# Kernel tuning notes

Measured on AMD Instinct MI355X. Metric: run time of the kernel, lower is better.

The kernel has to match this reference:

```python
import jax, jax.numpy as jnp
import numpy as np

NEG_BIG = -1.0e10
LRELU_SLOPE = 0.2
N_NODES = 256  # hardcoded in the original via np.identity(256)


def setup_inputs() -> dict:
    key = jax.random.key(0)
    ks = jax.random.split(key, 7)
    B, N, F, H, F_ = 128, N_NODES, 512, 8, 64
    X = jax.random.normal(ks[0], (B, N, F), dtype=jnp.float32)
    # binary adjacency mask in {0,1}
    A = jax.random.randint(ks[1], (B, N, N), 0, 2).astype(jnp.float32)
    kernels = jax.random.normal(ks[2], (H, F, F_), dtype=jnp.float32) * 0.05
    biases = jax.random.normal(ks[3], (H, F_), dtype=jnp.float32) * 0.05
    attn_self = jax.random.normal(ks[4], (H, F_), dtype=jnp.float32) * 0.05
    attn_neigh = jax.random.normal(ks[5], (H, F_), dtype=jnp.float32) * 0.05
    alpha = jax.random.normal(ks[6], (N // 2, N // 2), dtype=jnp.float32) * 0.05
    return {"X": X, "A": A, "kernels": kernels, "biases": biases,
            "attn_self": attn_self, "attn_neigh": attn_neigh, "alpha": alpha}


def reference(X, A, kernels, biases, attn_self, attn_neigh, alpha):
    B, N, F = X.shape
    H, _, F_ = kernels.shape
    # per-head linear projection: [H,B,N,F_]
    feats = jnp.einsum('bnf,hfk->hbnk', X, kernels)
    # additive attention logits
    a_self = jnp.einsum('hbnk,hk->hbn', feats, attn_self)    # [H,B,N]
    a_neigh = jnp.einsum('hbnk,hk->hbn', feats, attn_neigh)  # [H,B,N]
    dense = a_self[..., :, None] + a_neigh[..., None, :]     # [H,B,N,N]
    dense = jnp.where(dense > 0, dense, LRELU_SLOPE * dense)  # LeakyReLU(0.2)
    dense = dense + NEG_BIG * (1.0 - A)                      # mask non-edges
    attn = jax.nn.softmax(dense, axis=-1)                    # [H,B,N,N]
    # weighted aggregation + bias (dropout is identity at inference)
    node = jnp.einsum('hbij,hbjk->hbik', attn, feats) + biases[:, None, None, :]
    # concat heads -> [B,N,H*F_], then activation (relu)
    output = jnp.transpose(node, (1, 2, 0, 3)).reshape(B, N, H * F_)
    output = jax.nn.relu(output)

    # head-averaged attention map
    view = jnp.mean(attn, axis=0)                            # [B,N,N]
    # 2x2 max pool, stride 2
    pooled = view.reshape(B, N // 2, 2, N // 2, 2).max(axis=(2, 4))  # [B,N/2,N/2]
    temp = jnp.einsum('bij,jk->bik', pooled, alpha)
    s = jnp.sum(temp, axis=(-1, -2)).reshape(B, 1)           # [B,1]
    thresh = jax.nn.sigmoid(s)                               # [B,1]
    # binarize: where((view + I) < thresh, 1, 0), per-batch scalar threshold
    eye = jnp.eye(N, dtype=view.dtype)
    dense4 = jnp.where(view + eye[None] < thresh[:, :, None],
                       jnp.ones_like(view), jnp.zeros_like(view))
    return (output, dense4)
```

## Files before the change

### kernel.cpp

```cpp
#include <hip/hip_runtime.h>
#include <hip/hip_bf16.h>
#include <cstdio>
#include <math.h>


typedef __attribute__((ext_vector_type(8))) short   s16x8;
typedef __attribute__((ext_vector_type(8))) __bf16  bf16x8;
typedef __attribute__((ext_vector_type(4))) float   fx4;

#define FADD __fadd_rn
#define FMUL __fmul_rn
#define FSUB __fsub_rn
#define FDIV __fdiv_rn
#define MASKC (-9999998976.0f)

__device__ __forceinline__ fx4 mfma_bf16_16x16x32(s16x8 a, s16x8 b, fx4 c) {
    return __builtin_amdgcn_mfma_f32_16x16x32_bf16(
        __builtin_bit_cast(bf16x8, a), __builtin_bit_cast(bf16x8, b), c, 0, 0, 0);
}
__device__ __forceinline__ unsigned short f2bf(float f) {
    unsigned int x = __builtin_bit_cast(unsigned int, f);
    unsigned int lsb = (x >> 16) & 1u;
    x += 0x7fffu + lsb;
    return (unsigned short)(x >> 16);
}
__device__ __forceinline__ unsigned int pack2(float a, float b) {
    return (unsigned int)f2bf(a) | ((unsigned int)f2bf(b) << 16);
}
__device__ __forceinline__ float expf_cr(float x) {
    return (float)exp((double)x);
}

__device__ float pw128(const float* a) {
    float c[16];
#pragma unroll
    for (int l = 0; l < 16; ++l) {
        float t0 = FADD(FADD(a[l], a[16 + l]), FADD(a[32 + l], a[48 + l]));
        float t1 = FADD(FADD(a[64 + l], a[80 + l]), FADD(a[96 + l], a[112 + l]));
        c[l] = FADD(t0, t1);
    }
    float d[8], e[4], f[2];
#pragma unroll
    for (int l = 0; l < 8; ++l) d[l] = FADD(c[l], c[l + 8]);
#pragma unroll
    for (int l = 0; l < 4; ++l) e[l] = FADD(d[l], d[l + 4]);
#pragma unroll
    for (int l = 0; l < 2; ++l) f[l] = FADD(e[l], e[l + 2]);
    return FADD(f[0], f[1]);
}

__global__ __launch_bounds__(256) void repack_w(const float* __restrict__ kern,
                                                unsigned short* __restrict__ wkt) {
    int t = blockIdx.x * 256 + threadIdx.x;
    int n = t >> 9, f = t & 511;
    int h = n >> 6, k = n & 63;
    wkt[t] = f2bf(kern[(h * 512 + f) * 64 + k]);
}

__global__ __launch_bounds__(256) void repack_k32(const float* __restrict__ kern,
                                                  float* __restrict__ kern_r) {
    int t = blockIdx.x * 256 + threadIdx.x;
    int kk = t & 7, f = (t >> 3) & 511, kgh = t >> 12;
    int kg = kgh & 7, h = kgh >> 3;
    kern_r[t] = kern[(h * 512 + f) * 64 + kg * 8 + kk];
}

#define BK 32
__global__ __launch_bounds__(256) void gemm_feats(const float* __restrict__ X,
                                                  const unsigned short* __restrict__ Wkt,
                                                  unsigned short* __restrict__ feats_bf) {
    __shared__ alignas(16) unsigned short As[128 * BK];
    __shared__ alignas(16) unsigned short Bs[128 * BK];
    const int tid = threadIdx.x;
    const int mb = blockIdx.x >> 2, nb = blockIdx.x & 3;
    const int m0 = mb * 128, n0 = nb * 128;
    const int w = tid >> 6, lane = tid & 63;
    const int mw = (w & 1) * 64, nw = (w >> 1) * 64;
    const int lr = lane & 15, lq = lane >> 4;
    const int srow = tid >> 2, scol = (tid & 3) * 8;

    fx4 acc[4][4] = {};
    for (int k0 = 0; k0 < 512; k0 += BK) {
        __syncthreads();
        {
            const float* xr0 = &X[(m0 + srow) * 512 + k0 + scol];
            const float* xr1 = &X[(m0 + srow + 64) * 512 + k0 + scol];
            float4 a0 = *(const float4*)xr0, a1 = *(const float4*)(xr0 + 4);
            float4 b0 = *(const float4*)xr1, b1 = *(const float4*)(xr1 + 4);
            uint4 p0 = { pack2(a0.x, a0.y), pack2(a0.z, a0.w), pack2(a1.x, a1.y), pack2(a1.z, a1.w) };
            uint4 p1 = { pack2(b0.x, b0.y), pack2(b0.z, b0.w), pack2(b1.x, b1.y), pack2(b1.z, b1.w) };
            *(uint4*)&As[srow * BK + scol]        = p0;
            *(uint4*)&As[(srow + 64) * BK + scol] = p1;
            *(uint4*)&Bs[srow * BK + scol]        = *(const uint4*)&Wkt[(n0 + srow) * 512 + k0 + scol];
            *(uint4*)&Bs[(srow + 64) * BK + scol] = *(const uint4*)&Wkt[(n0 + srow + 64) * 512 + k0 + scol];
        }
        __syncthreads();
        s16x8 a[4], bb[4];
#pragma unroll
        for (int i = 0; i < 4; ++i) a[i]  = *(const s16x8*)&As[(mw + i * 16 + lr) * BK + lq * 8];
#pragma unroll
        for (int i = 0; i < 4; ++i) bb[i] = *(const s16x8*)&Bs[(nw + i * 16 + lr) * BK + lq * 8];
#pragma unroll
        for (int i = 0; i < 4; ++i)
#pragma unroll
            for (int j = 0; j < 4; ++j)
                acc[i][j] = mfma_bf16_16x16x32(a[i], bb[j], acc[i][j]);
    }
#pragma unroll
    for (int i = 0; i < 4; ++i)
#pragma unroll
        for (int j = 0; j < 4; ++j) {
            int col  = n0 + nw + j * 16 + lr;
            int rowb = m0 + mw + i * 16 + lq * 4;
#pragma unroll
            for (int r = 0; r < 4; ++r)
                feats_bf[(rowb + r) * 512 + col] = f2bf(acc[i][j][r]);
        }
}

#define FCH 128
#define XS_STRIDE 132
__global__ __launch_bounds__(512) void feats32_emu4(const float* __restrict__ X,
                                                    const float* __restrict__ kern_r,
                                                    float* __restrict__ feats32) {
    __shared__ alignas(16) float Xs[64 * XS_STRIDE];
    const int tid = threadIdx.x;
    const int hg = blockIdx.x >> 9;
    const int rb = blockIdx.x & 511;
    const int h0 = hg * 2;
    const int lane = tid & 63;
    const int kg = __builtin_amdgcn_readfirstlane(tid >> 6);
    const int k0 = kg * 8;
    const int row0 = rb * 64;
    const int srow = tid >> 3, sseg = tid & 7;

    float acc[2][8][4];
#pragma unroll
    for (int hh = 0; hh < 2; ++hh)
#pragma unroll
        for (int q = 0; q < 8; ++q)
#pragma unroll
            for (int l = 0; l < 4; ++l) acc[hh][q][l] = 0.f;

    const float* __restrict__ kp0 = &kern_r[(((h0 + 0) * 8 + kg) * 512) * 8];
    const float* __restrict__ kp1 = &kern_r[(((h0 + 1) * 8 + kg) * 512) * 8];

    for (int fc = 0; fc < 512; fc += FCH) {
        __syncthreads();
        {
            const float* gp = &X[(row0 + srow) * 512 + fc + sseg * 16];
            float* sp = &Xs[srow * XS_STRIDE + sseg * 16];
#pragma unroll
            for (int i = 0; i < 4; ++i)
                *(float4*)&sp[i * 4] = *(const float4*)&gp[i * 4];
        }
        __syncthreads();

        const float* __restrict__ xrow = &Xs[lane * XS_STRIDE];
        for (int fo = 0; fo < FCH; fo += 8) {
            float xv[8];
            {
                float4 xa = *(const float4*)&xrow[fo];
                float4 xb = *(const float4*)&xrow[fo + 4];
                xv[0] = xa.x; xv[1] = xa.y; xv[2] = xa.z; xv[3] = xa.w;
                xv[4] = xb.x; xv[5] = xb.y; xv[6] = xb.z; xv[7] = xb.w;
            }
#pragma unroll
            for (int hh = 0; hh < 2; ++hh) {
                const float* __restrict__ kp = (hh == 0 ? kp0 : kp1) + (fc + fo) * 8;
                float w[8][8];
#pragma unroll
                for (int j = 0; j < 8; ++j) {
                    float4 lo = *(const float4*)&kp[j * 8];
                    float4 hi = *(const float4*)&kp[j * 8 + 4];
                    w[j][0] = lo.x; w[j][1] = lo.y; w[j][2] = lo.z; w[j][3] = lo.w;
                    w[j][4] = hi.x; w[j][5] = hi.y; w[j][6] = hi.z; w[j][7] = hi.w;
                }
#pragma unroll
                for (int q = 0; q < 8; ++q) {
                    acc[hh][q][0] = FADD(acc[hh][q][0], FMUL(xv[0], w[0][q]));
                    acc[hh][q][1] = FADD(acc[hh][q][1], FMUL(xv[1], w[1][q]));
                    acc[hh][q][2] = FADD(acc[hh][q][2], FMUL(xv[2], w[2][q]));
                    acc[hh][q][3] = FADD(acc[hh][q][3], FMUL(xv[3], w[3][q]));
                    acc[hh][q][0] = FADD(acc[hh][q][0], FMUL(xv[4], w[4][q]));
                    acc[hh][q][1] = FADD(acc[hh][q][1], FMUL(xv[5], w[5][q]));
                    acc[hh][q][2] = FADD(acc[hh][q][2], FMUL(xv[6], w[6][q]));
                    acc[hh][q][3] = FADD(acc[hh][q][3], FMUL(xv[7], w[7][q]));
                }
            }
        }
    }

#pragma unroll
    for (int hh = 0; hh < 2; ++hh) {
        float* __restrict__ op = &feats32[((h0 + hh) * 32768 + row0 + lane) * 64 + k0];
        float4 o0, o1;
        o0.x = FADD(FADD(acc[hh][0][0], acc[hh][0][1]), FADD(acc[hh][0][2], acc[hh][0][3]));
        o0.y = FADD(FADD(acc[hh][1][0], acc[hh][1][1]), FADD(acc[hh][1][2], acc[hh][1][3]));
        o0.z = FADD(FADD(acc[hh][2][0], acc[hh][2][1]), FADD(acc[hh][2][2], acc[hh][2][3]));
        o0.w = FADD(FADD(acc[hh][3][0], acc[hh][3][1]), FADD(acc[hh][3][2], acc[hh][3][3]));
        o1.x = FADD(FADD(acc[hh][4][0], acc[hh][4][1]), FADD(acc[hh][4][2], acc[hh][4][3]));
        o1.y = FADD(FADD(acc[hh][5][0], acc[hh][5][1]), FADD(acc[hh][5][2], acc[hh][5][3]));
        o1.z = FADD(FADD(acc[hh][6][0], acc[hh][6][1]), FADD(acc[hh][6][2], acc[hh][6][3]));
        o1.w = FADD(FADD(acc[hh][7][0], acc[hh][7][1]), FADD(acc[hh][7][2], acc[hh][7][3]));
        *(float4*)&op[0] = o0;
        *(float4*)&op[4] = o1;
    }
}

__device__ float sse_dot64(const float* __restrict__ x, const float* __restrict__ y) {
    float a0 = 0.f, a1 = 0.f, a2 = 0.f, a3 = 0.f;
    for (int i = 0; i < 64; i += 8) {
        a0 = FADD(a0, FMUL(x[i + 0], y[i + 0]));
        a1 = FADD(a1, FMUL(x[i + 1], y[i + 1]));
        a2 = FADD(a2, FMUL(x[i + 2], y[i + 2]));
        a3 = FADD(a3, FMUL(x[i + 3], y[i + 3]));
        a0 = FADD(a0, FMUL(x[i + 4], y[i + 4]));
        a1 = FADD(a1, FMUL(x[i + 5], y[i + 5]));
        a2 = FADD(a2, FMUL(x[i + 6], y[i + 6]));
        a3 = FADD(a3, FMUL(x[i + 7], y[i + 7]));
    }
    return FADD(FADD(a0, a1), FADD(a2, a3));
}

__global__ __launch_bounds__(256) void logits_emu(const float* __restrict__ feats32,
                                                  const float* __restrict__ attn_s,
                                                  const float* __restrict__ attn_n,
                                                  float* __restrict__ a_s32,
                                                  float* __restrict__ a_n32) {
    int t = blockIdx.x * 256 + threadIdx.x;
    int row = t & 32767, h = t >> 15;
    const float* fr = &feats32[(h * 32768 + row) * 64];
    a_s32[h * 32768 + row] = sse_dot64(fr, &attn_s[h * 64]);
    a_n32[h * 32768 + row] = sse_dot64(fr, &attn_n[h * 64]);
}

#define VT_STRIDE 264
__global__ __launch_bounds__(256) void attn_emu(const float* __restrict__ A,
                                                const unsigned short* __restrict__ feats_bf,
                                                const float* __restrict__ a_s32,
                                                const float* __restrict__ a_n32,
                                                const float* __restrict__ biases,
                                                float* __restrict__ out0,
                                                float* __restrict__ view32) {
    __shared__ alignas(16) unsigned short Vt[64 * VT_STRIDE];
    __shared__ alignas(16) unsigned int   Abits[64][8];
    __shared__ alignas(16) float an_l[8][256];
    __shared__ alignas(16) float as_l[8][64];

    const int tid = threadIdx.x;
    const int b = blockIdx.x >> 2;
    const int row0 = (blockIdx.x & 3) * 64;
    const int w = tid >> 6, lane = tid & 63;
    const int m = lane & 15, jq = lane >> 4;

    {
        int i = tid >> 2, sg = tid & 3;
        const float* ar = &A[(((b << 8) + row0 + i) << 8) + sg * 64];
        unsigned int w0 = 0, w1 = 0;
#pragma unroll
        for (int q = 0; q < 8; ++q) {
            float4 av = *(const float4*)&ar[q * 4];
            unsigned int m4 = (av.x != 0.f ? 1u : 0u) | (av.y != 0.f ? 2u : 0u) |
                              (av.z != 0.f ? 4u : 0u) | (av.w != 0.f ? 8u : 0u);
            w0 |= m4 << (q * 4);
        }
#pragma unroll
        for (int q = 8; q < 16; ++q) {
            float4 av = *(const float4*)&ar[q * 4];
            unsigned int m4 = (av.x != 0.f ? 1u : 0u) | (av.y != 0.f ? 2u : 0u) |
                              (av.z != 0.f ? 4u : 0u) | (av.w != 0.f ? 8u : 0u);
            w1 |= m4 << ((q - 8) * 4);
        }
        Abits[i][sg * 2]     = w0;
        Abits[i][sg * 2 + 1] = w1;
    }
    for (int idx = tid; idx < 2048; idx += 256) {
        int h = idx >> 8, j = idx & 255;
        an_l[h][j] = a_n32[h * 32768 + (b << 8) + j];
    }
    for (int idx = tid; idx < 512; idx += 256) {
        int h = idx >> 6, i = idx & 63;
        as_l[h][i] = a_s32[h * 32768 + (b << 8) + row0 + i];
    }
    __syncthreads();

    const int i_ln = w * 16 + m;
    const int myrow = row0 + i_ln;
    unsigned int abits[8];
#pragma unroll
    for (int u = 0; u < 8; ++u) abits[u] = Abits[i_ln][u];

    float view_acc[8][8] = {};

    for (int h = 0; h < 8; ++h) {
        __syncthreads();
        {
            int jb = w;
#pragma unroll
            for (int it = 0; it < 8; ++it) {
                int j  = jb * 64 + it * 8 + (lane >> 3);
                int kg = lane & 7;
                s16x8 v8 = *(const s16x8*)&feats_bf[(((b << 8) + j) << 9) + (h << 6) + kg * 8];
#pragma unroll
                for (int u = 0; u < 8; ++u)
                    Vt[(kg * 8 + u) * VT_STRIDE + j] = (unsigned short)v8[u];
            }
        }
        __syncthreads();

        const float asv = as_l[h][i_ln];

        float ev[8][8];
        float Mloc = -3.4e38f;
#pragma unroll
        for (int kb = 0; kb < 8; ++kb) {
            int jbase = kb * 32 + jq * 8;
            float4 an0 = *(const float4*)&an_l[h][jbase];
            float4 an1 = *(const float4*)&an_l[h][jbase + 4];
            float anv[8] = { an0.x, an0.y, an0.z, an0.w, an1.x, an1.y, an1.z, an1.w };
            unsigned int mb = (abits[kb] >> (jq * 8)) & 0xffu;
#pragma unroll
            for (int t = 0; t < 8; ++t) {
                float lg = FADD(asv, anv[t]);
                float lr = lg > 0.f ? lg : FMUL(0.2f, lg);
                float v  = (mb & (1u << t)) ? lr : FADD(lr, MASKC);
                ev[kb][t] = v;
                Mloc = fmaxf(Mloc, v);
            }
        }
        Mloc = fmaxf(Mloc, __shfl_xor(Mloc, 16, 64));
        Mloc = fmaxf(Mloc, __shfl_xor(Mloc, 32, 64));
        const float Mi = Mloc;

#pragma unroll
        for (int kb = 0; kb < 8; ++kb)
#pragma unroll
            for (int t = 0; t < 8; ++t)
                ev[kb][t] = expf_cr(FSUB(ev[kb][t], Mi));

        float blkS[2];
#pragma unroll
        for (int blk = 0; blk < 2; ++blk) {
            float d[8];
#pragma unroll
            for (int t = 0; t < 8; ++t) {
                float s0 = FADD(ev[blk * 4 + 0][t], __shfl_xor(ev[blk * 4 + 0][t], 32, 64));
                float s1 = FADD(ev[blk * 4 + 1][t], __shfl_xor(ev[blk * 4 + 1][t], 32, 64));
                float s2 = FADD(ev[blk * 4 + 2][t], __shfl_xor(ev[blk * 4 + 2][t], 32, 64));
                float s3 = FADD(ev[blk * 4 + 3][t], __shfl_xor(ev[blk * 4 + 3][t], 32, 64));
                float cc = FADD(FADD(s0, s1), FADD(s2, s3));
                d[t] = FADD(cc, __shfl_xor(cc, 16, 64));
            }
            float e4[4], f2[2];
#pragma unroll
            for (int t = 0; t < 4; ++t) e4[t] = FADD(d[t], d[t + 4]);
            f2[0] = FADD(e4[0], e4[2]);
            f2[1] = FADD(e4[1], e4[3]);
            blkS[blk] = FADD(f2[0], f2[1]);
        }
        const float Si = FADD(blkS[0], blkS[1]);

        s16x8 pfrag[8];
#pragma unroll
        for (int kb = 0; kb < 8; ++kb) {
            s16x8 pf;
#pragma unroll
            for (int t = 0; t < 8; ++t) {
                float p = FDIV(ev[kb][t], Si);
                view_acc[kb][t] = FADD(view_acc[kb][t], FMUL(p, 0.125f));
                pf[t] = (short)f2bf(p);
            }
            pfrag[kb] = pf;
        }

        fx4 acc[4] = {};
#pragma unroll
        for (int kb = 0; kb < 8; ++kb) {
            int jo = kb * 32 + jq * 8;
#pragma unroll
            for (int nf = 0; nf < 4; ++nf) {
                s16x8 vf = *(const s16x8*)&Vt[(nf * 16 + m) * VT_STRIDE + jo];
                acc[nf] = mfma_bf16_16x16x32(pfrag[kb], vf, acc[nf]);
            }
        }
#pragma unroll
        for (int nf = 0; nf < 4; ++nf) {
            float bias = biases[h * 64 + nf * 16 + m];
#pragma unroll
            for (int r = 0; r < 4; ++r) {
                float val = acc[nf][r] + bias;
                val = val > 0.f ? val : 0.f;
                int gi = (b << 8) + row0 + w * 16 + jq * 4 + r;
                out0[gi * 512 + h * 64 + nf * 16 + m] = val;
            }
        }
    }

#pragma unroll
    for (int kb = 0; kb < 8; ++kb) {
        int base = (((b << 8) + myrow) << 8) + kb * 32 + jq * 8;
        float4 v0, v1;
        v0.x = view_acc[kb][0]; v0.y = view_acc[kb][1]; v0.z = view_acc[kb][2]; v0.w = view_acc[kb][3];
        v1.x = view_acc[kb][4]; v1.y = view_acc[kb][5]; v1.z = view_acc[kb][6]; v1.w = view_acc[kb][7];
        *(float4*)&view32[base]     = v0;
        *(float4*)&view32[base + 4] = v1;
    }
}

__global__ __launch_bounds__(256) void pool_emu(const float* __restrict__ view32,
                                                float* __restrict__ pooled) {
    int t = blockIdx.x * 256 + threadIdx.x;
    int j = t & 127, i = (t >> 7) & 127, b = t >> 14;
    const float* p = &view32[(b << 16) + (2 * i) * 256 + 2 * j];
    pooled[t] = fmaxf(fmaxf(p[0], p[1]), fmaxf(p[256], p[257]));
}

__global__ __launch_bounds__(256) void temp_emu(const float* __restrict__ pooled,
                                                const float* __restrict__ alpha,
                                                float* __restrict__ temp) {
    int t = blockIdx.x * 256 + threadIdx.x;
    int k = t & 127, i = (t >> 7) & 127, b = t >> 14;
    const float* pr = &pooled[(b << 14) + i * 128];
    const float* ap = &alpha[k];
    float a0 = 0.f, a1 = 0.f, a2 = 0.f, a3 = 0.f;
    for (int j = 0; j < 128; j += 8) {
        a0 = FADD(a0, FMUL(pr[j + 0], ap[(j + 0) * 128]));
        a1 = FADD(a1, FMUL(pr[j + 1], ap[(j + 1) * 128]));
        a2 = FADD(a2, FMUL(pr[j + 2], ap[(j + 2) * 128]));
        a3 = FADD(a3, FMUL(pr[j + 3], ap[(j + 3) * 128]));
        a0 = FADD(a0, FMUL(pr[j + 4], ap[(j + 4) * 128]));
        a1 = FADD(a1, FMUL(pr[j + 5], ap[(j + 5) * 128]));
        a2 = FADD(a2, FMUL(pr[j + 6], ap[(j + 6) * 128]));
        a3 = FADD(a3, FMUL(pr[j + 7], ap[(j + 7) * 128]));
    }
    temp[t] = FADD(FADD(a0, a1), FADD(a2, a3));
}

__global__ __launch_bounds__(128) void thresh_emu(const float* __restrict__ temp,
                                                  float* __restrict__ thresh32) {
    __shared__ float red[128];
    int l = threadIdx.x, b = blockIdx.x;
    red[l] = pw128(&temp[(b << 14) + l * 128]);
    __syncthreads();
    for (int s = 64; s >= 1; s >>= 1) {
        float v = 0.f;
        if (l < s) v = FADD(red[2 * l], red[2 * l + 1]);
        __syncthreads();
        if (l < s) red[l] = v;
        __syncthreads();
    }
    if (l == 0) {
        float sfin = red[0];
        float e = expf_cr(-sfin);
        thresh32[b] = FDIV(1.0f, FADD(1.0f, e));
    }
}

__global__ __launch_bounds__(256) void binarize_emu(const float* __restrict__ view32,
                                                    const float* __restrict__ thresh32,
                                                    float* __restrict__ out1) {
    int g = blockIdx.x * 256 + threadIdx.x;
    int e = g * 4;
    int b = e >> 16, i = (e >> 8) & 255, j = e & 255;
    float th = thresh32[b];
    float4 v = *(const float4*)&view32[e];
    float4 o;
    o.x = (FADD(v.x, (i == j + 0) ? 1.f : 0.f) < th) ? 1.f : 0.f;
    o.y = (FADD(v.y, (i == j + 1) ? 1.f : 0.f) < th) ? 1.f : 0.f;
    o.z = (FADD(v.z, (i == j + 2) ? 1.f : 0.f) < th) ? 1.f : 0.f;
    o.w = (FADD(v.w, (i == j + 3) ? 1.f : 0.f) < th) ? 1.f : 0.f;
    *(float4*)&out1[e] = o;
}

static inline void ck_launch(const char* name) {
    hipError_t e = hipGetLastError();
    if (e != hipSuccess)
        fprintf(stderr, "[gat] %s launch error %d: %s\n", name, (int)e, hipGetErrorString(e));
}

extern "C" void kernel_launch(void* const* d_in, const int* in_sizes, int n_in,
                              void* d_out, int out_size, void* d_ws, size_t ws_size,
                              hipStream_t stream) {
    const float* X      = (const float*)d_in[0];
    const float* A      = (const float*)d_in[1];
    const float* kern   = (const float*)d_in[2];
    const float* biases = (const float*)d_in[3];
    const float* attn_s = (const float*)d_in[4];
    const float* attn_n = (const float*)d_in[5];
    const float* alpha  = (const float*)d_in[6];

    char* ws = (char*)d_ws;
    unsigned short* feats_bf = (unsigned short*)(ws);
    float*          feats32  = (float*)(ws + 33554432);
    float*          view32   = (float*)(ws + 100663296);
    float*          a_s32    = (float*)(ws + 134217728);
    float*          a_n32    = (float*)(ws + 135266304);
    float*          pooled   = (float*)(ws + 136314880);
    float*          temp     = (float*)(ws + 144703488);
    float*          thresh32 = (float*)(ws + 153092096);
    unsigned short* wkt      = (unsigned short*)(ws + 153092608);

    float*          kern_r   = (float*)(ws + 100663296);

    float* out0 = (float*)d_out;
    float* out1 = out0 + 16777216;

    repack_w    <<<1024, 256, 0, stream>>>(kern, wkt);              ck_launch("repack_w");
    repack_k32  <<<1024, 256, 0, stream>>>(kern, kern_r);           ck_launch("repack_k32");
    gemm_feats  <<<1024, 256, 0, stream>>>(X, wkt, feats_bf);       ck_launch("gemm_feats");
    feats32_emu4<<<2048, 512, 0, stream>>>(X, kern_r, feats32);     ck_launch("feats32_emu4");
    logits_emu  <<<1024, 256, 0, stream>>>(feats32, attn_s, attn_n, a_s32, a_n32);
                                                                    ck_launch("logits_emu");
    attn_emu    <<<512, 256, 0, stream>>>(A, feats_bf, a_s32, a_n32, biases, out0, view32);
                                                                    ck_launch("attn_emu");
    pool_emu    <<<8192, 256, 0, stream>>>(view32, pooled);         ck_launch("pool_emu");
    temp_emu    <<<8192, 256, 0, stream>>>(pooled, alpha, temp);    ck_launch("temp_emu");
    thresh_emu  <<<128, 128, 0, stream>>>(temp, thresh32);          ck_launch("thresh_emu");
    binarize_emu<<<8192, 256, 0, stream>>>(view32, thresh32, out1); ck_launch("binarize_emu");
}
```

Baseline: 706.3 us.

## Use packed fp32 math and double-buffered LDS in fp32 feature projection

Rewrites the exact-fp32 feature projection kernel so each lane keeps its accumulators as float2 pairs, aiming for packed fp32 multiply and add instructions. The weight repack interleaves pairs of adjacent input features to match that layout. The X tile now goes through two LDS buffers: the next chunk is read from global memory while the current chunk is computed, which removes one barrier per chunk. The summation order is kept identical and contraction is turned off to preserve bitwise emulation, at the cost of higher register pressure.

```diff
diff --git a/kernel.cpp b/kernel.cpp
--- a/kernel.cpp
+++ b/kernel.cpp
@@ -7,6 +7,7 @@
 typedef __attribute__((ext_vector_type(8))) short   s16x8;
 typedef __attribute__((ext_vector_type(8))) __bf16  bf16x8;
 typedef __attribute__((ext_vector_type(4))) float   fx4;
+typedef __attribute__((ext_vector_type(2))) float   fx2;
 
 #define FADD __fadd_rn
 #define FMUL __fmul_rn
@@ -57,12 +58,16 @@
     wkt[t] = f2bf(kern[(h * 512 + f) * 64 + k]);
 }
 
-__global__ __launch_bounds__(256) void repack_k32(const float* __restrict__ kern,
-                                                  float* __restrict__ kern_r) {
+__global__ __launch_bounds__(256) void repack_k32p(const float* __restrict__ kern,
+                                                   float* __restrict__ kern_r2) {
     int t = blockIdx.x * 256 + threadIdx.x;
-    int kk = t & 7, f = (t >> 3) & 511, kgh = t >> 12;
+    int e  = t & 1;
+    int q  = (t >> 1) & 7;
+    int fp = (t >> 4) & 255;
+    int kgh = t >> 12;
     int kg = kgh & 7, h = kgh >> 3;
-    kern_r[t] = kern[(h * 512 + f) * 64 + kg * 8 + kk];
+    int f = fp * 2 + e;
+    kern_r2[t] = kern[(h * 512 + f) * 64 + kg * 8 + q];
 }
 
 #define BK 32
@@ -118,12 +123,13 @@
         }
 }
 
-#define FCH 128
-#define XS_STRIDE 132
-__global__ __launch_bounds__(512) void feats32_emu4(const float* __restrict__ X,
-                                                    const float* __restrict__ kern_r,
+#define FCH2 64
+#define XS2_STRIDE 68
+__global__ __launch_bounds__(512) void feats32_emu5(const float* __restrict__ X,
+                                                    const float* __restrict__ kern_r2,
                                                     float* __restrict__ feats32) {
-    __shared__ alignas(16) float Xs[64 * XS_STRIDE];
+#pragma clang fp contract(off)
+    __shared__ alignas(16) float Xs[2][64 * XS2_STRIDE];
     const int tid = threadIdx.x;
     const int hg = blockIdx.x >> 9;
     const int rb = blockIdx.x & 511;
@@ -134,75 +140,83 @@
     const int row0 = rb * 64;
     const int srow = tid >> 3, sseg = tid & 7;
 
-    float acc[2][8][4];
+    fx2 acc01[2][8];
+    fx2 acc23[2][8];
 #pragma unroll
     for (int hh = 0; hh < 2; ++hh)
 #pragma unroll
-        for (int q = 0; q < 8; ++q)
-#pragma unroll
-            for (int l = 0; l < 4; ++l) acc[hh][q][l] = 0.f;
-
-    const float* __restrict__ kp0 = &kern_r[(((h0 + 0) * 8 + kg) * 512) * 8];
-    const float* __restrict__ kp1 = &kern_r[(((h0 + 1) * 8 + kg) * 512) * 8];
-
-    for (int fc = 0; fc < 512; fc += FCH) {
-        __syncthreads();
-        {
-            const float* gp = &X[(row0 + srow) * 512 + fc + sseg * 16];
-            float* sp = &Xs[srow * XS_STRIDE + sseg * 16];
-#pragma unroll
-            for (int i = 0; i < 4; ++i)
-                *(float4*)&sp[i * 4] = *(const float4*)&gp[i * 4];
-        }
-        __syncthreads();
-
-        const float* __restrict__ xrow = &Xs[lane * XS_STRIDE];
-        for (int fo = 0; fo < FCH; fo += 8) {
-            float xv[8];
-            {
-                float4 xa = *(const float4*)&xrow[fo];
-                float4 xb = *(const float4*)&xrow[fo + 4];
-                xv[0] = xa.x; xv[1] = xa.y; xv[2] = xa.z; xv[3] = xa.w;
-                xv[4] = xb.x; xv[5] = xb.y; xv[6] = xb.z; xv[7] = xb.w;
-            }
+        for (int q = 0; q < 8; ++q) {
+            acc01[hh][q] = (fx2)(0.f);
+            acc23[hh][q] = (fx2)(0.f);
+        }
+
+    const float* __restrict__ kp0 = &kern_r2[(((h0 + 0) * 8 + kg) * 256) * 16];
+    const float* __restrict__ kp1 = &kern_r2[(((h0 + 1) * 8 + kg) * 256) * 16];
+
+    float4 nx0, nx1;
+    {
+        const float* gp = &X[(row0 + srow) * 512 + sseg * 8];
+        nx0 = *(const float4*)gp; nx1 = *(const float4*)(gp + 4);
+        *(float4*)&Xs[0][srow * XS2_STRIDE + sseg * 8]     = nx0;
+        *(float4*)&Xs[0][srow * XS2_STRIDE + sseg * 8 + 4] = nx1;
+    }
+    __syncthreads();
+
+    for (int ch = 0; ch < 8; ++ch) {
+        const int fc = ch * FCH2;
+        const int cur = ch & 1;
+        if (ch < 7) {
+            const float* gp = &X[(row0 + srow) * 512 + fc + FCH2 + sseg * 8];
+            nx0 = *(const float4*)gp; nx1 = *(const float4*)(gp + 4);
+        }
+
+        const float* __restrict__ xrow = &Xs[cur][lane * XS2_STRIDE];
+#pragma unroll
+        for (int fo = 0; fo < FCH2; fo += 8) {
+            float4 xa = *(const float4*)&xrow[fo];
+            float4 xb = *(const float4*)&xrow[fo + 4];
+            fx2 x01; x01.x = xa.x; x01.y = xa.y;
+            fx2 x23; x23.x = xa.z; x23.y = xa.w;
+            fx2 x45; x45.x = xb.x; x45.y = xb.y;
+            fx2 x67; x67.x = xb.z; x67.y = xb.w;
+            const int fp0 = (fc + fo) >> 1;
 #pragma unroll
             for (int hh = 0; hh < 2; ++hh) {
-                const float* __restrict__ kp = (hh == 0 ? kp0 : kp1) + (fc + fo) * 8;
-                float w[8][8];
-#pragma unroll
-                for (int j = 0; j < 8; ++j) {
-                    float4 lo = *(const float4*)&kp[j * 8];
-                    float4 hi = *(const float4*)&kp[j * 8 + 4];
-                    w[j][0] = lo.x; w[j][1] = lo.y; w[j][2] = lo.z; w[j][3] = lo.w;
-                    w[j][4] = hi.x; w[j][5] = hi.y; w[j][6] = hi.z; w[j][7] = hi.w;
+                const fx2* __restrict__ wv =
+                    (const fx2*)((hh == 0 ? kp0 : kp1) + fp0 * 16);
+#pragma unroll
+                for (int q = 0; q < 8; ++q) {
+                    fx2 m0 = x01 * wv[q];
+                    acc01[hh][q] = acc01[hh][q] + m0;
+                    fx2 m1 = x45 * wv[16 + q];
+                    acc01[hh][q] = acc01[hh][q] + m1;
+                    fx2 m2 = x23 * wv[8 + q];
+                    acc23[hh][q] = acc23[hh][q] + m2;
+                    fx2 m3 = x67 * wv[24 + q];
+                    acc23[hh][q] = acc23[hh][q] + m3;
                 }
-#pragma unroll
-                for (int q = 0; q < 8; ++q) {
-                    acc[hh][q][0] = FADD(acc[hh][q][0], FMUL(xv[0], w[0][q]));
-                    acc[hh][q][1] = FADD(acc[hh][q][1], FMUL(xv[1], w[1][q]));
-                    acc[hh][q][2] = FADD(acc[hh][q][2], FMUL(xv[2], w[2][q]));
-                    acc[hh][q][3] = FADD(acc[hh][q][3], FMUL(xv[3], w[3][q]));
-                    acc[hh][q][0] = FADD(acc[hh][q][0], FMUL(xv[4], w[4][q]));
-                    acc[hh][q][1] = FADD(acc[hh][q][1], FMUL(xv[5], w[5][q]));
-                    acc[hh][q][2] = FADD(acc[hh][q][2], FMUL(xv[6], w[6][q]));
-                    acc[hh][q][3] = FADD(acc[hh][q][3], FMUL(xv[7], w[7][q]));
-                }
-            }
-        }
+            }
+        }
+
+        if (ch < 7) {
+            *(float4*)&Xs[cur ^ 1][srow * XS2_STRIDE + sseg * 8]     = nx0;
+            *(float4*)&Xs[cur ^ 1][srow * XS2_STRIDE + sseg * 8 + 4] = nx1;
+        }
+        __syncthreads();
     }
 
 #pragma unroll
     for (int hh = 0; hh < 2; ++hh) {
         float* __restrict__ op = &feats32[((h0 + hh) * 32768 + row0 + lane) * 64 + k0];
         float4 o0, o1;
-        o0.x = FADD(FADD(acc[hh][0][0], acc[hh][0][1]), FADD(acc[hh][0][2], acc[hh][0][3]));
-        o0.y = FADD(FADD(acc[hh][1][0], acc[hh][1][1]), FADD(acc[hh][1][2], acc[hh][1][3]));
-        o0.z = FADD(FADD(acc[hh][2][0], acc[hh][2][1]), FADD(acc[hh][2][2], acc[hh][2][3]));
-        o0.w = FADD(FADD(acc[hh][3][0], acc[hh][3][1]), FADD(acc[hh][3][2], acc[hh][3][3]));
-        o1.x = FADD(FADD(acc[hh][4][0], acc[hh][4][1]), FADD(acc[hh][4][2], acc[hh][4][3]));
-        o1.y = FADD(FADD(acc[hh][5][0], acc[hh][5][1]), FADD(acc[hh][5][2], acc[hh][5][3]));
-        o1.z = FADD(FADD(acc[hh][6][0], acc[hh][6][1]), FADD(acc[hh][6][2], acc[hh][6][3]));
-        o1.w = FADD(FADD(acc[hh][7][0], acc[hh][7][1]), FADD(acc[hh][7][2], acc[hh][7][3]));
+        o0.x = FADD(FADD(acc01[hh][0].x, acc01[hh][0].y), FADD(acc23[hh][0].x, acc23[hh][0].y));
+        o0.y = FADD(FADD(acc01[hh][1].x, acc01[hh][1].y), FADD(acc23[hh][1].x, acc23[hh][1].y));
+        o0.z = FADD(FADD(acc01[hh][2].x, acc01[hh][2].y), FADD(acc23[hh][2].x, acc23[hh][2].y));
+        o0.w = FADD(FADD(acc01[hh][3].x, acc01[hh][3].y), FADD(acc23[hh][3].x, acc23[hh][3].y));
+        o1.x = FADD(FADD(acc01[hh][4].x, acc01[hh][4].y), FADD(acc23[hh][4].x, acc23[hh][4].y));
+        o1.y = FADD(FADD(acc01[hh][5].x, acc01[hh][5].y), FADD(acc23[hh][5].x, acc23[hh][5].y));
+        o1.z = FADD(FADD(acc01[hh][6].x, acc01[hh][6].y), FADD(acc23[hh][6].x, acc23[hh][6].y));
+        o1.w = FADD(FADD(acc01[hh][7].x, acc01[hh][7].y), FADD(acc23[hh][7].x, acc23[hh][7].y));
         *(float4*)&op[0] = o0;
         *(float4*)&op[4] = o1;
     }
@@ -501,15 +515,15 @@
     float*          thresh32 = (float*)(ws + 153092096);
     unsigned short* wkt      = (unsigned short*)(ws + 153092608);
 
-    float*          kern_r   = (float*)(ws + 100663296);
+    float*          kern_r2  = (float*)(ws + 100663296);
 
     float* out0 = (float*)d_out;
     float* out1 = out0 + 16777216;
 
     repack_w    <<<1024, 256, 0, stream>>>(kern, wkt);              ck_launch("repack_w");
-    repack_k32  <<<1024, 256, 0, stream>>>(kern, kern_r);           ck_launch("repack_k32");
+    repack_k32p <<<1024, 256, 0, stream>>>(kern, kern_r2);          ck_launch("repack_k32p");
     gemm_feats  <<<1024, 256, 0, stream>>>(X, wkt, feats_bf);       ck_launch("gemm_feats");
-    feats32_emu4<<<2048, 512, 0, stream>>>(X, kern_r, feats32);     ck_launch("feats32_emu4");
+    feats32_emu5<<<2048, 512, 0, stream>>>(X, kern_r2, feats32);    ck_launch("feats32_emu5");
     logits_emu  <<<1024, 256, 0, stream>>>(feats32, attn_s, attn_n, a_s32, a_n32);
                                                                     ck_launch("logits_emu");
     attn_emu    <<<512, 256, 0, stream>>>(A, feats_bf, a_s32, a_n32, biases, out0, view32);
```

After: 1.877 ms. +165.7%, slower.
